# Kernel optimization log

Hardware: AMD Instinct MI355X
Metric: run time of the kernel (lower is better)

The kernel has to match this reference:

```python
import jax, jax.numpy as jnp
import numpy as np
from jax import lax

B, N, C = 16, 2304, 768
H_HEADS, D = 12, 64  # num_heads, head_dim
SCALE = 9.0 ** (-0.5)  # equivalent_head_dim ** -0.5


def setup_inputs() -> dict:
    key = jax.random.key(0)
    ks = jax.random.split(key, 8)
    return {
        "x": jax.random.normal(ks[0], (B, N, C), dtype=jnp.float32),
        "qkv_w": jax.random.normal(ks[1], (3 * C + 3 * D, C), dtype=jnp.float32) * 0.02,
        "qkv_b": jax.random.normal(ks[2], (3 * C + 3 * D,), dtype=jnp.float32) * 0.02,
        "w1": jax.random.normal(ks[3], (1, H_HEADS, D, D), dtype=jnp.float32) * 0.02,
        "w2": jax.random.normal(ks[4], (1, H_HEADS, D, D), dtype=jnp.float32) * 0.02,
        "w3": jax.random.normal(ks[5], (D, 1, 3, 3), dtype=jnp.float32) * 0.02,
        "proj_w": jax.random.normal(ks[6], (C, C + D), dtype=jnp.float32) * 0.02,
        "proj_b": jax.random.normal(ks[7], (C,), dtype=jnp.float32) * 0.02,
        "h": 48,
        "w": 48,
    }


def _inner_swiglu(k, v, w1, w2, lr=1.0):
    # k, v: [B, H, N, d]; w1, w2: [1, H, d, d]
    z1 = jnp.einsum('bhnd,hde->bhne', k, w1[0])
    z2 = jnp.einsum('bhnd,hde->bhne', k, w2[0])
    sig = jax.nn.sigmoid(z2)
    a = z2 * sig
    e = -v / float(v.shape[2]) * SCALE
    g1 = jnp.einsum('bhnd,bhne->bhde', k, e * a)
    g2 = jnp.einsum('bhnd,bhne->bhde', k, e * z1 * (sig * (1.0 + z2 * (1.0 - sig))))
    g1 = g1 / (jnp.linalg.norm(g1, axis=-2, keepdims=True) + 1.0)
    g2 = g2 / (jnp.linalg.norm(g2, axis=-2, keepdims=True) + 1.0)
    return w1 - lr * g1, w2 - lr * g2  # [B, H, d, d]


def _inner_3x3dwc(k, v, w3, hh, ww, lr=1.0):
    # k, v: [B, d, h, w]; w3: [d, 1, 3, 3]
    b, c = k.shape[0], k.shape[1]
    e = -v / float(hh * ww) * SCALE
    kp = jnp.pad(k, ((0, 0), (0, 0), (1, 1), (1, 1)))
    dots = []
    for ys in (0, 1, 2):  # 1 + dy
        for xs in (0, 1, 2):  # 1 + dx
            dots.append(jnp.sum(kp[:, :, ys:ys + hh, xs:xs + ww] * e, axis=(-2, -1)))
    g = jnp.stack(dots, axis=-1).reshape(b * c, 1, 3, 3)
    g = g / (jnp.sqrt(jnp.sum(g * g, axis=(-2, -1), keepdims=True)) + 1.0)
    return jnp.tile(w3, (b, 1, 1, 1)) - lr * g  # [B*d, 1, 3, 3]


def reference(x, qkv_w, qkv_b, w1, w2, w3, proj_w, proj_b, h, w):
    b, n, c = x.shape
    nh = w1.shape[1]
    d = c // nh
    qkv = x @ qkv_w.T + qkv_b  # [B, N, 3C + 3d]
    q1, k1, v1, q2, k2, v2 = jnp.split(
        qkv, [c, 2 * c, 3 * c, 3 * c + d, 3 * c + 2 * d], axis=-1)
    heads = lambda t: t.reshape(b, n, nh, d).transpose(0, 2, 1, 3)
    q1, k1, v1 = heads(q1), heads(k1), heads(v1)

    w1u, w2u = _inner_swiglu(k1, v1, w1, w2)
    x1 = jnp.einsum('bhnd,bhde->bhne', q1, w1u) * jax.nn.silu(
        jnp.einsum('bhnd,bhde->bhne', q1, w2u))
    x1 = x1.transpose(0, 2, 1, 3).reshape(b, n, c)

    spatial = lambda t: t.reshape(b, h, w, d).transpose(0, 3, 1, 2)  # [B, d, h, w]
    q2s, k2s, v2s = spatial(q2), spatial(k2), spatial(v2)
    w3u = _inner_3x3dwc(k2s, v2s, w3, h, w)
    x2 = lax.conv_general_dilated(
        q2s.reshape(1, b * d, h, w), w3u,
        window_strides=(1, 1), padding=((1, 1), (1, 1)),
        feature_group_count=b * d,
        dimension_numbers=('NCHW', 'OIHW', 'NCHW'))
    x2 = x2.reshape(b, d, n).transpose(0, 2, 1)  # [B, N, d]

    out = jnp.concatenate([x1, x2], axis=-1) @ proj_w.T + proj_b
    return out
```

## Files before the change

### kernel.cpp

```cpp
#include <hip/hip_runtime.h>
#include <hip/hip_bf16.h>
#include <math.h>

#define B_   16
#define N_   2304
#define C_   768
#define H_   12
#define D_   64
#define M_   (B_*N_)
#define NQKV 2496
#define NPAD 2560
#define CCP  896
#define EVS  (-1.0f/6912.0f)

typedef __bf16 bf16x8 __attribute__((ext_vector_type(8)));
typedef __bf16 bf16x4 __attribute__((ext_vector_type(4)));
typedef float  f32x4  __attribute__((ext_vector_type(4)));

static __device__ __forceinline__ void gload_lds16(const void* g, void* l) {
  __builtin_amdgcn_global_load_lds((const __attribute__((address_space(1))) void*)g,
                                   (__attribute__((address_space(3))) void*)l, 16, 0, 0);
}

static __device__ __forceinline__ bf16x8 ld8(const __bf16* p) {
  bf16x4 lo = *(const bf16x4*)p;
  bf16x4 hi = *(const bf16x4*)(p + 4);
  return __builtin_shufflevector(lo, hi, 0,1,2,3,4,5,6,7);
}

__global__ __launch_bounds__(256) void cvt_x(const float* __restrict__ in,
                                             __bf16* __restrict__ out, int n8) {
  int i = blockIdx.x * 256 + threadIdx.x;
  if (i >= n8) return;
  const float4* p = (const float4*)(in + (size_t)i * 8);
  float4 a = p[0], b = p[1];
  bf16x8 o = {(__bf16)a.x,(__bf16)a.y,(__bf16)a.z,(__bf16)a.w,
              (__bf16)b.x,(__bf16)b.y,(__bf16)b.z,(__bf16)b.w};
  *(bf16x8*)(out + (size_t)i * 8) = o;
}

__global__ __launch_bounds__(256) void cvt_wqkv(const float* __restrict__ w,
    const float* __restrict__ bias, __bf16* __restrict__ wout, float* __restrict__ bout) {
  int i = blockIdx.x * 256 + threadIdx.x;
  if (i < NPAD * 96) {
    int n = i / 96, c8 = i - n * 96;
    bf16x8 o;
    if (n < NQKV) {
      const float4* p = (const float4*)(w + (size_t)n * 768 + c8 * 8);
      float4 a = p[0], b = p[1];
      o = (bf16x8){(__bf16)a.x,(__bf16)a.y,(__bf16)a.z,(__bf16)a.w,
                   (__bf16)b.x,(__bf16)b.y,(__bf16)b.z,(__bf16)b.w};
    } else {
      o = (bf16x8){(__bf16)0.f,(__bf16)0.f,(__bf16)0.f,(__bf16)0.f,
                   (__bf16)0.f,(__bf16)0.f,(__bf16)0.f,(__bf16)0.f};
    }
    *(bf16x8*)(wout + (size_t)n * 768 + c8 * 8) = o;
  }
  if (i < NPAD) bout[i] = (i < NQKV) ? bias[i] : 0.0f;
}

__global__ __launch_bounds__(256) void cvt_pw(const float* __restrict__ in,
                                              __bf16* __restrict__ out) {
  int i = blockIdx.x * 256 + threadIdx.x;
  if (i >= 86016) return;
  int n = i / 112, c8 = i - n * 112;
  int k = c8 * 8;
  bf16x8 o;
  if (k < 832) {
    const float4* p = (const float4*)(in + (size_t)n * 832 + k);
    float4 a = p[0], b = p[1];
    o = (bf16x8){(__bf16)a.x,(__bf16)a.y,(__bf16)a.z,(__bf16)a.w,
                 (__bf16)b.x,(__bf16)b.y,(__bf16)b.z,(__bf16)b.w};
  } else {
    o = (bf16x8){(__bf16)0.f,(__bf16)0.f,(__bf16)0.f,(__bf16)0.f,
                 (__bf16)0.f,(__bf16)0.f,(__bf16)0.f,(__bf16)0.f};
  }
  *(bf16x8*)(out + (size_t)n * CCP + k) = o;
}

__global__ __launch_bounds__(256) void zeropad(__bf16* __restrict__ concat) {
  int i = blockIdx.x * 256 + threadIdx.x;
  if (i >= M_ * 8) return;
  int row = i >> 3, ch = i & 7;
  bf16x8 z = {(__bf16)0.f,(__bf16)0.f,(__bf16)0.f,(__bf16)0.f,
              (__bf16)0.f,(__bf16)0.f,(__bf16)0.f,(__bf16)0.f};
  *(bf16x8*)(concat + (size_t)row * CCP + 832 + ch * 8) = z;
}

template<int OUTF32>
__global__ __launch_bounds__(512, 2) void gemm8(
    const __bf16* __restrict__ A, const __bf16* __restrict__ Bt,
    const float* __restrict__ bias, void* __restrict__ Cout,
    const int K, const int ldc, const int nbn, const int KT)
{
  __shared__ __align__(16) __bf16 sA[2][2][128 * 64];
  __shared__ __align__(16) __bf16 sB[2][2][128 * 64];
  const int tid  = threadIdx.x;
  const int lane = tid & 63;
  const int wid  = tid >> 6;
  const int wm = wid >> 2;
  const int wn = wid & 3;
  const int l15 = lane & 15, lq = lane >> 4;

  const int nwg = gridDim.x;
  const int swz = ((int)blockIdx.x & 7) * (nwg >> 3) + ((int)blockIdx.x >> 3);
  const int bm = swz / nbn;
  const int bn = swz - bm * nbn;

  const int strow = tid >> 3;
  const int stoff = strow * 64 + (tid & 7) * 8;
  const __bf16* gA = A  + (size_t)((size_t)bm * 256 + strow) * K + ((tid & 7) ^ (strow & 7)) * 8;
  const __bf16* gB = Bt + (size_t)((size_t)bn * 256 + strow) * K + ((tid & 7) ^ (strow & 7)) * 8;

  f32x4 acc[2][4][2][2];
  #pragma unroll
  for (int a = 0; a < 2; ++a)
    #pragma unroll
    for (int m = 0; m < 4; ++m)
      #pragma unroll
      for (int b = 0; b < 2; ++b)
        #pragma unroll
        for (int n = 0; n < 2; ++n) acc[a][m][b][n] = (f32x4){0.f,0.f,0.f,0.f};

  bf16x8 af0[4][2], af1[4][2], bf0[2][2], bf1[2][2];

#define STAGE_A(q, h, T) do {                                                   \
    const size_t ko_ = (size_t)(T) * 64;                                        \
    gload_lds16(gA + (size_t)((h)*128 +  0) * K + ko_, &sA[q][h][stoff]);       \
    gload_lds16(gA + (size_t)((h)*128 + 64) * K + ko_, &sA[q][h][4096 + stoff]);\
  } while (0)
#define STAGE_B(q, h, T) do {                                                   \
    const size_t ko_ = (size_t)(T) * 64;                                        \
    gload_lds16(gB + (size_t)((h)*128 +  0) * K + ko_, &sB[q][h][stoff]);       \
    gload_lds16(gB + (size_t)((h)*128 + 64) * K + ko_, &sB[q][h][4096 + stoff]);\
  } while (0)
#define LOADA(DST, h, q) do {                                                   \
    _Pragma("unroll") for (int mf_ = 0; mf_ < 4; ++mf_) {                       \
      const int r_ = wm * 64 + mf_ * 16 + l15;                                  \
      _Pragma("unroll") for (int kk_ = 0; kk_ < 2; ++kk_)                       \
        DST[mf_][kk_] = *(const bf16x8*)&sA[q][h][r_ * 64 + (((kk_*4+lq) ^ (r_&7)) * 8)]; \
    } } while (0)
#define LOADB(DST, h, q) do {                                                   \
    _Pragma("unroll") for (int nf_ = 0; nf_ < 2; ++nf_) {                       \
      const int c_ = wn * 32 + nf_ * 16 + l15;                                  \
      _Pragma("unroll") for (int kk_ = 0; kk_ < 2; ++kk_)                       \
        DST[nf_][kk_] = *(const bf16x8*)&sB[q][h][c_ * 64 + (((kk_*4+lq) ^ (c_&7)) * 8)]; \
    } } while (0)
#define MMA(a_, b_, AF, BF) do {                                                \
    __builtin_amdgcn_s_setprio(1);                                              \
    _Pragma("unroll") for (int kk_ = 0; kk_ < 2; ++kk_)                         \
    _Pragma("unroll") for (int mf_ = 0; mf_ < 4; ++mf_)                         \
    _Pragma("unroll") for (int nf_ = 0; nf_ < 2; ++nf_)                         \
      acc[a_][mf_][b_][nf_] = __builtin_amdgcn_mfma_f32_16x16x32_bf16(          \
          AF[mf_][kk_], BF[nf_][kk_], acc[a_][mf_][b_][nf_], 0, 0, 0);          \
    __builtin_amdgcn_s_setprio(0);                                              \
  } while (0)
#define BAR  do { __builtin_amdgcn_s_barrier();                                 \
                  __builtin_amdgcn_sched_barrier(0); } while (0)
#define VMW4 do { asm volatile("s_waitcnt vmcnt(4)" ::: "memory");              \
                  __builtin_amdgcn_sched_barrier(0); } while (0)
#define VMW0 do { asm volatile("s_waitcnt vmcnt(0)" ::: "memory");              \
                  __builtin_amdgcn_sched_barrier(0); } while (0)

  STAGE_A(0, 0, 0); STAGE_A(0, 1, 0); STAGE_B(0, 0, 0); STAGE_B(0, 1, 0);
  STAGE_B(1, 0, 1);
  STAGE_A(1, 1, 1);
  VMW4;
  BAR;

  for (int t = 0; t < KT; t += 2) {
    LOADA(af0, 0, 0); LOADB(bf0, 0, 0);
    STAGE_A(1, 0, t + 1); STAGE_B(1, 1, t + 1);
    BAR; MMA(0, 0, af0, bf0); BAR;
    LOADA(af1, 1, 0);
    BAR; MMA(1, 0, af1, bf0); BAR;
    LOADB(bf1, 1, 0);
    if (t + 2 < KT) STAGE_B(0, 0, t + 2);
    BAR; MMA(1, 1, af1, bf1); BAR;
    if (t + 2 < KT) STAGE_A(0, 1, t + 2);
    BAR; MMA(0, 1, af0, bf1);
    if (t + 2 < KT) { VMW4; } else { VMW0; }
    BAR;
    LOADA(af0, 0, 1); LOADB(bf0, 0, 1);
    if (t + 2 < KT) { STAGE_A(0, 0, t + 2); STAGE_B(0, 1, t + 2); }
    BAR; MMA(0, 0, af0, bf0); BAR;
    LOADA(af1, 1, 1);
    BAR; MMA(1, 0, af1, bf0); BAR;
    LOADB(bf1, 1, 1);
    if (t + 3 < KT) STAGE_B(1, 0, t + 3);
    BAR; MMA(1, 1, af1, bf1); BAR;
    if (t + 3 < KT) STAGE_A(1, 1, t + 3);
    BAR; MMA(0, 1, af0, bf1);
    if (t + 3 < KT) { VMW4; } else { VMW0; }
    BAR;
  }
#undef STAGE_A
#undef STAGE_B
#undef LOADA
#undef LOADB
#undef MMA

  #pragma unroll
  for (int b = 0; b < 2; ++b)
    #pragma unroll
    for (int nf = 0; nf < 2; ++nf) {
      const int col = bn * 256 + b * 128 + wn * 32 + nf * 16 + l15;
      const float bs = bias[col];
      #pragma unroll
      for (int a = 0; a < 2; ++a)
        #pragma unroll
        for (int mf = 0; mf < 4; ++mf) {
          const int row0 = bm * 256 + a * 128 + wm * 64 + mf * 16 + lq * 4;
          #pragma unroll
          for (int r = 0; r < 4; ++r) {
            float v = acc[a][mf][b][nf][r] + bs;
            if (OUTF32) ((float*)Cout)[(size_t)(row0 + r) * ldc + col] = v;
            else        ((__bf16*)Cout)[(size_t)(row0 + r) * ldc + col] = (__bf16)v;
          }
        }
    }
}

__global__ __launch_bounds__(512, 1) void inner_swiglu(
    const __bf16* __restrict__ qkv, const float* __restrict__ w1,
    const float* __restrict__ w2, __bf16* __restrict__ concat)
{
  const int bh = blockIdx.x;
  const int b = bh / H_, h = bh - b * H_;
  const int tid = threadIdx.x, wid = tid >> 6, lane = tid & 63;
  const int grp = wid >> 2;
  const int wid2 = wid & 3;
  const int wr = wid2 >> 1, wc = wid2 & 1, l15 = lane & 15, lq = lane >> 4;

  __shared__ __bf16 w1T[64 * 72], w2T[64 * 72];
  __shared__ union U {
    struct { __bf16 kN[2][64 * 72], kT[2][64 * 72], vN[2][64 * 72],
                    t1T[2][64 * 72], t2T[2][64 * 72]; } c;
    struct { float g1[64 * 65], g2[64 * 65]; float nrm1[64], nrm2[64]; } g;
  } u;

  const float* w1p = w1 + h * 4096;
  const float* w2p = w2 + h * 4096;
  for (int idx = tid; idx < 4096; idx += 512) {
    int d = idx >> 6, e = idx & 63;
    w1T[e * 72 + d] = (__bf16)w1p[idx];
    w2T[e * 72 + d] = (__bf16)w2p[idx];
  }

  f32x4 g1a[2][2], g2a[2][2];
  #pragma unroll
  for (int i = 0; i < 2; ++i)
    #pragma unroll
    for (int j = 0; j < 2; ++j) { g1a[i][j] = (f32x4){0.f,0.f,0.f,0.f}; g2a[i][j] = (f32x4){0.f,0.f,0.f,0.f}; }

  const size_t rowb = (size_t)b * N_;
  const int koff = C_ + h * D_;
  const int voff = 2 * C_ + h * D_;
  const int st = tid & 255, sn = st >> 2, sdb = st & 3;

  for (int it = 0; it < 18; ++it) {
    const int n0 = (it * 2 + grp) * 64;
    {
      const __bf16* src = qkv + (rowb + n0 + sn) * (size_t)NPAD + koff + sdb * 16;
      bf16x8 va = *(const bf16x8*)src;
      bf16x8 vb = *(const bf16x8*)(src + 8);
      __bf16* kn = &u.c.kN[grp][sn * 72 + sdb * 16];
      *(bf16x4*)(kn + 0)  = __builtin_shufflevector(va, va, 0,1,2,3);
      *(bf16x4*)(kn + 4)  = __builtin_shufflevector(va, va, 4,5,6,7);
      *(bf16x4*)(kn + 8)  = __builtin_shufflevector(vb, vb, 0,1,2,3);
      *(bf16x4*)(kn + 12) = __builtin_shufflevector(vb, vb, 4,5,6,7);
      #pragma unroll
      for (int j = 0; j < 8; ++j) u.c.kT[grp][(sdb * 16 + j) * 72 + sn] = va[j];
      #pragma unroll
      for (int j = 0; j < 8; ++j) u.c.kT[grp][(sdb * 16 + 8 + j) * 72 + sn] = vb[j];
      const __bf16* vsrc = qkv + (rowb + n0 + sn) * (size_t)NPAD + voff + sdb * 16;
      bf16x8 wa = *(const bf16x8*)vsrc;
      bf16x8 wb = *(const bf16x8*)(vsrc + 8);
      __bf16* vn = &u.c.vN[grp][sn * 72 + sdb * 16];
      *(bf16x4*)(vn + 0)  = __builtin_shufflevector(wa, wa, 0,1,2,3);
      *(bf16x4*)(vn + 4)  = __builtin_shufflevector(wa, wa, 4,5,6,7);
      *(bf16x4*)(vn + 8)  = __builtin_shufflevector(wb, wb, 0,1,2,3);
      *(bf16x4*)(vn + 12) = __builtin_shufflevector(wb, wb, 4,5,6,7);
    }
    __syncthreads();

    f32x4 z1[2][2], z2[2][2];
    #pragma unroll
    for (int i = 0; i < 2; ++i)
      #pragma unroll
      for (int j = 0; j < 2; ++j) { z1[i][j] = (f32x4){0.f,0.f,0.f,0.f}; z2[i][j] = (f32x4){0.f,0.f,0.f,0.f}; }
    #pragma unroll
    for (int kk = 0; kk < 2; ++kk) {
      bf16x8 af[2], b1[2], b2[2];
      #pragma unroll
      for (int mi = 0; mi < 2; ++mi)
        af[mi] = ld8(&u.c.kN[grp][(wr * 32 + mi * 16 + l15) * 72 + kk * 32 + lq * 8]);
      #pragma unroll
      for (int ni = 0; ni < 2; ++ni) {
        int e = wc * 32 + ni * 16 + l15;
        b1[ni] = ld8(&w1T[e * 72 + kk * 32 + lq * 8]);
        b2[ni] = ld8(&w2T[e * 72 + kk * 32 + lq * 8]);
      }
      #pragma unroll
      for (int mi = 0; mi < 2; ++mi)
        #pragma unroll
        for (int ni = 0; ni < 2; ++ni) {
          z1[mi][ni] = __builtin_amdgcn_mfma_f32_16x16x32_bf16(af[mi], b1[ni], z1[mi][ni], 0, 0, 0);
          z2[mi][ni] = __builtin_amdgcn_mfma_f32_16x16x32_bf16(af[mi], b2[ni], z2[mi][ni], 0, 0, 0);
        }
    }

    #pragma unroll
    for (int mi = 0; mi < 2; ++mi)
      #pragma unroll
      for (int ni = 0; ni < 2; ++ni) {
        int nl = wr * 32 + mi * 16 + lq * 4;
        int e  = wc * 32 + ni * 16 + l15;
        #pragma unroll
        for (int r = 0; r < 4; ++r) {
          float vv  = (float)u.c.vN[grp][(nl + r) * 72 + e];
          float ev  = vv * EVS;
          float z1v = z1[mi][ni][r], z2v = z2[mi][ni][r];
          float sg  = 1.0f / (1.0f + __expf(-z2v));
          float t1  = ev * (z2v * sg);
          float t2  = ev * z1v * (sg * (1.0f + z2v * (1.0f - sg)));
          u.c.t1T[grp][e * 72 + nl + r] = (__bf16)t1;
          u.c.t2T[grp][e * 72 + nl + r] = (__bf16)t2;
        }
      }
    __syncthreads();

    #pragma unroll
    for (int kk = 0; kk < 2; ++kk) {
      bf16x8 af[2], b1[2], b2[2];
      #pragma unroll
      for (int mi = 0; mi < 2; ++mi)
        af[mi] = ld8(&u.c.kT[grp][(wr * 32 + mi * 16 + l15) * 72 + kk * 32 + lq * 8]);
      #pragma unroll
      for (int ni = 0; ni < 2; ++ni) {
        int e = wc * 32 + ni * 16 + l15;
        b1[ni] = ld8(&u.c.t1T[grp][e * 72 + kk * 32 + lq * 8]);
        b2[ni] = ld8(&u.c.t2T[grp][e * 72 + kk * 32 + lq * 8]);
      }
      #pragma unroll
      for (int mi = 0; mi < 2; ++mi)
        #pragma unroll
        for (int ni = 0; ni < 2; ++ni) {
          g1a[mi][ni] = __builtin_amdgcn_mfma_f32_16x16x32_bf16(af[mi], b1[ni], g1a[mi][ni], 0, 0, 0);
          g2a[mi][ni] = __builtin_amdgcn_mfma_f32_16x16x32_bf16(af[mi], b2[ni], g2a[mi][ni], 0, 0, 0);
        }
    }
    __syncthreads();
  }

  if (grp == 0) {
    #pragma unroll
    for (int mi = 0; mi < 2; ++mi)
      #pragma unroll
      for (int ni = 0; ni < 2; ++ni)
        #pragma unroll
        for (int r = 0; r < 4; ++r) {
          int d = wr * 32 + mi * 16 + lq * 4 + r;
          int e = wc * 32 + ni * 16 + l15;
          u.g.g1[d * 65 + e] = g1a[mi][ni][r];
          u.g.g2[d * 65 + e] = g2a[mi][ni][r];
        }
  }
  __syncthreads();
  if (grp == 1) {
    #pragma unroll
    for (int mi = 0; mi < 2; ++mi)
      #pragma unroll
      for (int ni = 0; ni < 2; ++ni)
        #pragma unroll
        for (int r = 0; r < 4; ++r) {
          int d = wr * 32 + mi * 16 + lq * 4 + r;
          int e = wc * 32 + ni * 16 + l15;
          u.g.g1[d * 65 + e] += g1a[mi][ni][r];
          u.g.g2[d * 65 + e] += g2a[mi][ni][r];
        }
  }
  __syncthreads();
  if (tid < 128) {
    const float* gs = (tid < 64) ? u.g.g1 : u.g.g2;
    int e = tid & 63;
    float s = 0.f;
    for (int d = 0; d < 64; ++d) { float gv = gs[d * 65 + e]; s += gv * gv; }
    float rn = 1.0f / (sqrtf(s) + 1.0f);
    if (tid < 64) u.g.nrm1[e] = rn; else u.g.nrm2[e] = rn;
  }
  __syncthreads();
  for (int idx = tid; idx < 4096; idx += 512) {
    int d = idx >> 6, e = idx & 63;
    float wu1 = w1p[idx] - u.g.g1[d * 65 + e] * u.g.nrm1[e];
    float wu2 = w2p[idx] - u.g.g2[d * 65 + e] * u.g.nrm2[e];
    w1T[e * 72 + d] = (__bf16)wu1;
    w2T[e * 72 + d] = (__bf16)wu2;
  }
  __syncthreads();

  const int qoff = h * D_;
  for (int it = 0; it < 18; ++it) {
    const int n0 = (it * 2 + grp) * 64;
    {
      const __bf16* src = qkv + (rowb + n0 + sn) * (size_t)NPAD + qoff + sdb * 16;
      bf16x8 va = *(const bf16x8*)src;
      bf16x8 vb = *(const bf16x8*)(src + 8);
      __bf16* kn = &u.c.kN[grp][sn * 72 + sdb * 16];
      *(bf16x4*)(kn + 0)  = __builtin_shufflevector(va, va, 0,1,2,3);
      *(bf16x4*)(kn + 4)  = __builtin_shufflevector(va, va, 4,5,6,7);
      *(bf16x4*)(kn + 8)  = __builtin_shufflevector(vb, vb, 0,1,2,3);
      *(bf16x4*)(kn + 12) = __builtin_shufflevector(vb, vb, 4,5,6,7);
    }
    __syncthreads();
    f32x4 y1[2][2], y2[2][2];
    #pragma unroll
    for (int i = 0; i < 2; ++i)
      #pragma unroll
      for (int j = 0; j < 2; ++j) { y1[i][j] = (f32x4){0.f,0.f,0.f,0.f}; y2[i][j] = (f32x4){0.f,0.f,0.f,0.f}; }
    #pragma unroll
    for (int kk = 0; kk < 2; ++kk) {
      bf16x8 af[2], b1[2], b2[2];
      #pragma unroll
      for (int mi = 0; mi < 2; ++mi)
        af[mi] = ld8(&u.c.kN[grp][(wr * 32 + mi * 16 + l15) * 72 + kk * 32 + lq * 8]);
      #pragma unroll
      for (int ni = 0; ni < 2; ++ni) {
        int e = wc * 32 + ni * 16 + l15;
        b1[ni] = ld8(&w1T[e * 72 + kk * 32 + lq * 8]);
        b2[ni] = ld8(&w2T[e * 72 + kk * 32 + lq * 8]);
      }
      #pragma unroll
      for (int mi = 0; mi < 2; ++mi)
        #pragma unroll
        for (int ni = 0; ni < 2; ++ni) {
          y1[mi][ni] = __builtin_amdgcn_mfma_f32_16x16x32_bf16(af[mi], b1[ni], y1[mi][ni], 0, 0, 0);
          y2[mi][ni] = __builtin_amdgcn_mfma_f32_16x16x32_bf16(af[mi], b2[ni], y2[mi][ni], 0, 0, 0);
        }
    }
    #pragma unroll
    for (int mi = 0; mi < 2; ++mi)
      #pragma unroll
      for (int ni = 0; ni < 2; ++ni) {
        int nl = wr * 32 + mi * 16 + lq * 4;
        int e  = wc * 32 + ni * 16 + l15;
        #pragma unroll
        for (int r = 0; r < 4; ++r) {
          float a1 = y1[mi][ni][r], a2 = y2[mi][ni][r];
          float sg = 1.0f / (1.0f + __expf(-a2));
          concat[(rowb + n0 + nl + r) * (size_t)CCP + h * D_ + e] = (__bf16)(a1 * (a2 * sg));
        }
      }
    __syncthreads();
  }
}

__global__ __launch_bounds__(256) void dwc_grad2(const __bf16* __restrict__ qkv,
                                                 float* __restrict__ w3p) {
  const int blk = blockIdx.x;
  const int b = blk / 12, sp = blk - b * 12;
  const int tid = threadIdx.x, dd = tid & 63, rl = tid >> 6;
  __shared__ __bf16 kS[6 * 50 * 64];
  __shared__ float red[4][9][64];
  for (int i = tid; i < 9600; i += 256) ((unsigned*)kS)[i] = 0u;
  __syncthreads();
  const size_t base = (size_t)b * N_ * NPAD;
  for (int i = tid; i < 6 * 48 * 8; i += 256) {
    int y6 = i / 384; int rem = i - y6 * 384; int x = rem >> 3; int c8 = rem & 7;
    int y = 4 * sp - 1 + y6;
    if (y >= 0 && y < 48) {
      int p = y * 48 + x;
      bf16x8 v = *(const bf16x8*)&qkv[base + (size_t)p * NPAD + 2368 + c8 * 8];
      *(bf16x8*)&kS[((y6 * 50) + x + 1) * 64 + c8 * 8] = v;
    }
  }
  __syncthreads();
  float acc[9];
  #pragma unroll
  for (int j = 0; j < 9; ++j) acc[j] = 0.f;
  const int y = 4 * sp + rl;
  for (int x = 0; x < 48; ++x) {
    int p = y * 48 + x;
    float e = (float)qkv[base + (size_t)p * NPAD + 2432 + dd] * EVS;
    #pragma unroll
    for (int j = 0; j < 9; ++j) {
      int ys = j / 3, xs = j - ys * 3;
      acc[j] += (float)kS[((rl + ys) * 50 + x + xs) * 64 + dd] * e;
    }
  }
  #pragma unroll
  for (int j = 0; j < 9; ++j) red[rl][j][dd] = acc[j];
  __syncthreads();
  if (rl == 0) {
    #pragma unroll
    for (int j = 0; j < 9; ++j) {
      float s = red[0][j][dd] + red[1][j][dd] + red[2][j][dd] + red[3][j][dd];
      w3p[((size_t)(b * 12 + sp) * 64 + dd) * 9 + j] = s;
    }
  }
}

__global__ __launch_bounds__(256) void dwc_upd(const float* __restrict__ w3p,
    const float* __restrict__ w3, float* __restrict__ w3u) {
  int i = blockIdx.x * 256 + threadIdx.x;
  if (i >= 1024) return;
  int b = i >> 6, dd = i & 63;
  float g[9];
  #pragma unroll
  for (int j = 0; j < 9; ++j) g[j] = 0.f;
  for (int sp = 0; sp < 12; ++sp)
    #pragma unroll
    for (int j = 0; j < 9; ++j)
      g[j] += w3p[((size_t)(b * 12 + sp) * 64 + dd) * 9 + j];
  float ss = 0.f;
  #pragma unroll
  for (int j = 0; j < 9; ++j) ss += g[j] * g[j];
  float rn = 1.0f / (sqrtf(ss) + 1.0f);
  #pragma unroll
  for (int j = 0; j < 9; ++j) w3u[i * 9 + j] = w3[dd * 9 + j] - g[j] * rn;
}

__global__ __launch_bounds__(256) void dwc_apply2(const __bf16* __restrict__ qkv,
    const float* __restrict__ w3u, __bf16* __restrict__ concat) {
  const int blk = blockIdx.x;
  const int b = blk / 12, sp = blk - b * 12;
  const int tid = threadIdx.x, dd = tid & 63, rl = tid >> 6;
  __shared__ __bf16 qS[6 * 50 * 64];
  for (int i = tid; i < 9600; i += 256) ((unsigned*)qS)[i] = 0u;
  __syncthreads();
  const size_t base = (size_t)b * N_ * NPAD;
  for (int i = tid; i < 6 * 48 * 8; i += 256) {
    int y6 = i / 384; int rem = i - y6 * 384; int x = rem >> 3; int c8 = rem & 7;
    int y = 4 * sp - 1 + y6;
    if (y >= 0 && y < 48) {
      int p = y * 48 + x;
      bf16x8 v = *(const bf16x8*)&qkv[base + (size_t)p * NPAD + 2304 + c8 * 8];
      *(bf16x8*)&qS[((y6 * 50) + x + 1) * 64 + c8 * 8] = v;
    }
  }
  __syncthreads();
  float wv[9];
  #pragma unroll
  for (int j = 0; j < 9; ++j) wv[j] = w3u[(size_t)(b * 64 + dd) * 9 + j];
  const int y = 4 * sp + rl;
  for (int x = 0; x < 48; ++x) {
    float s = 0.f;
    #pragma unroll
    for (int j = 0; j < 9; ++j) {
      int ys = j / 3, xs = j - ys * 3;
      s += (float)qS[((rl + ys) * 50 + x + xs) * 64 + dd] * wv[j];
    }
    int p = y * 48 + x;
    concat[((size_t)b * N_ + p) * CCP + 768 + dd] = (__bf16)s;
  }
}

extern "C" void kernel_launch(void* const* d_in, const int* in_sizes, int n_in,
                              void* d_out, int out_size, void* d_ws, size_t ws_size,
                              hipStream_t stream) {
  const float* x      = (const float*)d_in[0];
  const float* qkv_w  = (const float*)d_in[1];
  const float* qkv_b  = (const float*)d_in[2];
  const float* w1     = (const float*)d_in[3];
  const float* w2     = (const float*)d_in[4];
  const float* w3     = (const float*)d_in[5];
  const float* proj_w = (const float*)d_in[6];
  const float* proj_b = (const float*)d_in[7];

  char* ws = (char*)d_ws;
  __bf16* xb     = (__bf16*)ws;
  __bf16* wqkvb  = (__bf16*)(ws + 56623104);
  float*  qkvbp  = (float*) (ws + 60555264);
  __bf16* concat = (__bf16*)ws;
  __bf16* qkvb16 = (__bf16*)(ws + 66060288);
  __bf16* pwb    = (__bf16*)(ws + 254803968);
  float*  w3u    = (float*) (ws + 256180224);
  float*  w3p    = (float*) (ws + 256217088);

  cvt_x   <<<13824, 256, 0, stream>>>(x, xb, 3538944);
  cvt_wqkv<<<  960, 256, 0, stream>>>(qkv_w, qkv_b, wqkvb, qkvbp);
  cvt_pw  <<<  336, 256, 0, stream>>>(proj_w, pwb);

  gemm8<0><<<1440, 512, 0, stream>>>(xb, wqkvb, qkvbp, (void*)qkvb16,
                                     768, NPAD, 10, 12);

  zeropad<<<1152, 256, 0, stream>>>(concat);
  inner_swiglu<<<192, 512, 0, stream>>>(qkvb16, w1, w2, concat);
  dwc_grad2 <<<192, 256, 0, stream>>>(qkvb16, w3p);
  dwc_upd   <<<  4, 256, 0, stream>>>(w3p, w3, w3u);
  dwc_apply2<<<192, 256, 0, stream>>>(qkvb16, w3u, concat);

  gemm8<1><<<432, 512, 0, stream>>>(concat, pwb, proj_b, d_out,
                                    CCP, 768, 3, 14);
}
```

Baseline: 453.2 us.

## Replace 256x256 ping-pong GEMM with simpler 128x128 double-buffered GEMM

Swaps the 8-wave 256x256-tile GEMM, which had an interleaved ping-pong schedule of barriers, priorities and partial waits, for a 4-wave 128x128-tile kernel. The new kernel uses a plain double-buffered LDS loop that prefetches the next K-tile and waits with vmcnt(0) before each barrier. Launching four times as many workgroups should give better occupancy and wave balance across CUs. In exchange it loses data reuse per tile, doubling global and LDS traffic per FLOP, and it drops the fine-grained overlap of loads and MFMA.

```diff
diff --git a/kernel.cpp b/kernel.cpp
--- a/kernel.cpp
+++ b/kernel.cpp
@@ -88,18 +88,17 @@
 }
 
 template<int OUTF32>
-__global__ __launch_bounds__(512, 2) void gemm8(
+__global__ __launch_bounds__(256, 2) void gemmP(
     const __bf16* __restrict__ A, const __bf16* __restrict__ Bt,
     const float* __restrict__ bias, void* __restrict__ Cout,
     const int K, const int ldc, const int nbn, const int KT)
 {
-  __shared__ __align__(16) __bf16 sA[2][2][128 * 64];
-  __shared__ __align__(16) __bf16 sB[2][2][128 * 64];
+  __shared__ __align__(16) __bf16 sA[2][128 * 64];
+  __shared__ __align__(16) __bf16 sB[2][128 * 64];
   const int tid  = threadIdx.x;
   const int lane = tid & 63;
   const int wid  = tid >> 6;
-  const int wm = wid >> 2;
-  const int wn = wid & 3;
+  const int wm = wid >> 1, wn = wid & 1;
   const int l15 = lane & 15, lq = lane >> 4;
 
   const int nwg = gridDim.x;
@@ -109,116 +108,75 @@
 
   const int strow = tid >> 3;
   const int stoff = strow * 64 + (tid & 7) * 8;
-  const __bf16* gA = A  + (size_t)((size_t)bm * 256 + strow) * K + ((tid & 7) ^ (strow & 7)) * 8;
-  const __bf16* gB = Bt + (size_t)((size_t)bn * 256 + strow) * K + ((tid & 7) ^ (strow & 7)) * 8;
-
-  f32x4 acc[2][4][2][2];
-  #pragma unroll
-  for (int a = 0; a < 2; ++a)
-    #pragma unroll
-    for (int m = 0; m < 4; ++m)
-      #pragma unroll
-      for (int b = 0; b < 2; ++b)
-        #pragma unroll
-        for (int n = 0; n < 2; ++n) acc[a][m][b][n] = (f32x4){0.f,0.f,0.f,0.f};
-
-  bf16x8 af0[4][2], af1[4][2], bf0[2][2], bf1[2][2];
-
-#define STAGE_A(q, h, T) do {                                                   \
+  const __bf16* gA = A  + (size_t)((size_t)bm * 128 + strow) * K + ((tid & 7) ^ (strow & 7)) * 8;
+  const __bf16* gB = Bt + (size_t)((size_t)bn * 128 + strow) * K + ((tid & 7) ^ (strow & 7)) * 8;
+
+  f32x4 acc[4][4];
+  #pragma unroll
+  for (int m = 0; m < 4; ++m)
+    #pragma unroll
+    for (int n = 0; n < 4; ++n) acc[m][n] = (f32x4){0.f,0.f,0.f,0.f};
+
+#define STAGE(q, T) do {                                                        \
     const size_t ko_ = (size_t)(T) * 64;                                        \
-    gload_lds16(gA + (size_t)((h)*128 +  0) * K + ko_, &sA[q][h][stoff]);       \
-    gload_lds16(gA + (size_t)((h)*128 + 64) * K + ko_, &sA[q][h][4096 + stoff]);\
-  } while (0)
-#define STAGE_B(q, h, T) do {                                                   \
-    const size_t ko_ = (size_t)(T) * 64;                                        \
-    gload_lds16(gB + (size_t)((h)*128 +  0) * K + ko_, &sB[q][h][stoff]);       \
-    gload_lds16(gB + (size_t)((h)*128 + 64) * K + ko_, &sB[q][h][4096 + stoff]);\
-  } while (0)
-#define LOADA(DST, h, q) do {                                                   \
-    _Pragma("unroll") for (int mf_ = 0; mf_ < 4; ++mf_) {                       \
-      const int r_ = wm * 64 + mf_ * 16 + l15;                                  \
-      _Pragma("unroll") for (int kk_ = 0; kk_ < 2; ++kk_)                       \
-        DST[mf_][kk_] = *(const bf16x8*)&sA[q][h][r_ * 64 + (((kk_*4+lq) ^ (r_&7)) * 8)]; \
+    _Pragma("unroll")                                                           \
+    for (int j_ = 0; j_ < 4; ++j_) {                                            \
+      gload_lds16(gA + (size_t)(j_ * 32) * K + ko_, &sA[q][j_ * 2048 + stoff]); \
+      gload_lds16(gB + (size_t)(j_ * 32) * K + ko_, &sB[q][j_ * 2048 + stoff]); \
     } } while (0)
-#define LOADB(DST, h, q) do {                                                   \
-    _Pragma("unroll") for (int nf_ = 0; nf_ < 2; ++nf_) {                       \
-      const int c_ = wn * 32 + nf_ * 16 + l15;                                  \
-      _Pragma("unroll") for (int kk_ = 0; kk_ < 2; ++kk_)                       \
-        DST[nf_][kk_] = *(const bf16x8*)&sB[q][h][c_ * 64 + (((kk_*4+lq) ^ (c_&7)) * 8)]; \
-    } } while (0)
-#define MMA(a_, b_, AF, BF) do {                                                \
-    __builtin_amdgcn_s_setprio(1);                                              \
-    _Pragma("unroll") for (int kk_ = 0; kk_ < 2; ++kk_)                         \
-    _Pragma("unroll") for (int mf_ = 0; mf_ < 4; ++mf_)                         \
-    _Pragma("unroll") for (int nf_ = 0; nf_ < 2; ++nf_)                         \
-      acc[a_][mf_][b_][nf_] = __builtin_amdgcn_mfma_f32_16x16x32_bf16(          \
-          AF[mf_][kk_], BF[nf_][kk_], acc[a_][mf_][b_][nf_], 0, 0, 0);          \
-    __builtin_amdgcn_s_setprio(0);                                              \
-  } while (0)
-#define BAR  do { __builtin_amdgcn_s_barrier();                                 \
-                  __builtin_amdgcn_sched_barrier(0); } while (0)
-#define VMW4 do { asm volatile("s_waitcnt vmcnt(4)" ::: "memory");              \
-                  __builtin_amdgcn_sched_barrier(0); } while (0)
-#define VMW0 do { asm volatile("s_waitcnt vmcnt(0)" ::: "memory");              \
-                  __builtin_amdgcn_sched_barrier(0); } while (0)
-
-  STAGE_A(0, 0, 0); STAGE_A(0, 1, 0); STAGE_B(0, 0, 0); STAGE_B(0, 1, 0);
-  STAGE_B(1, 0, 1);
-  STAGE_A(1, 1, 1);
-  VMW4;
-  BAR;
-
-  for (int t = 0; t < KT; t += 2) {
-    LOADA(af0, 0, 0); LOADB(bf0, 0, 0);
-    STAGE_A(1, 0, t + 1); STAGE_B(1, 1, t + 1);
-    BAR; MMA(0, 0, af0, bf0); BAR;
-    LOADA(af1, 1, 0);
-    BAR; MMA(1, 0, af1, bf0); BAR;
-    LOADB(bf1, 1, 0);
-    if (t + 2 < KT) STAGE_B(0, 0, t + 2);
-    BAR; MMA(1, 1, af1, bf1); BAR;
-    if (t + 2 < KT) STAGE_A(0, 1, t + 2);
-    BAR; MMA(0, 1, af0, bf1);
-    if (t + 2 < KT) { VMW4; } else { VMW0; }
-    BAR;
-    LOADA(af0, 0, 1); LOADB(bf0, 0, 1);
-    if (t + 2 < KT) { STAGE_A(0, 0, t + 2); STAGE_B(0, 1, t + 2); }
-    BAR; MMA(0, 0, af0, bf0); BAR;
-    LOADA(af1, 1, 1);
-    BAR; MMA(1, 0, af1, bf0); BAR;
-    LOADB(bf1, 1, 1);
-    if (t + 3 < KT) STAGE_B(1, 0, t + 3);
-    BAR; MMA(1, 1, af1, bf1); BAR;
-    if (t + 3 < KT) STAGE_A(1, 1, t + 3);
-    BAR; MMA(0, 1, af0, bf1);
-    if (t + 3 < KT) { VMW4; } else { VMW0; }
-    BAR;
-  }
-#undef STAGE_A
-#undef STAGE_B
-#undef LOADA
-#undef LOADB
-#undef MMA
-
-  #pragma unroll
-  for (int b = 0; b < 2; ++b)
-    #pragma unroll
-    for (int nf = 0; nf < 2; ++nf) {
-      const int col = bn * 256 + b * 128 + wn * 32 + nf * 16 + l15;
-      const float bs = bias[col];
-      #pragma unroll
-      for (int a = 0; a < 2; ++a)
-        #pragma unroll
-        for (int mf = 0; mf < 4; ++mf) {
-          const int row0 = bm * 256 + a * 128 + wm * 64 + mf * 16 + lq * 4;
-          #pragma unroll
-          for (int r = 0; r < 4; ++r) {
-            float v = acc[a][mf][b][nf][r] + bs;
-            if (OUTF32) ((float*)Cout)[(size_t)(row0 + r) * ldc + col] = v;
-            else        ((__bf16*)Cout)[(size_t)(row0 + r) * ldc + col] = (__bf16)v;
-          }
-        }
-    }
+
+  STAGE(0, 0);
+  asm volatile("s_waitcnt vmcnt(0)" ::: "memory");
+  __builtin_amdgcn_s_barrier();
+
+  for (int t = 0; t < KT; ++t) {
+    const int q = t & 1;
+    if (t + 1 < KT) STAGE(q ^ 1, t + 1);
+
+    bf16x8 af[4][2], bf[4][2];
+    #pragma unroll
+    for (int mf = 0; mf < 4; ++mf) {
+      const int r = wm * 64 + mf * 16 + l15;
+      #pragma unroll
+      for (int kk = 0; kk < 2; ++kk)
+        af[mf][kk] = *(const bf16x8*)&sA[q][r * 64 + (((kk * 4 + lq) ^ (r & 7)) * 8)];
+    }
+    #pragma unroll
+    for (int nf = 0; nf < 4; ++nf) {
+      const int c = wn * 64 + nf * 16 + l15;
+      #pragma unroll
+      for (int kk = 0; kk < 2; ++kk)
+        bf[nf][kk] = *(const bf16x8*)&sB[q][c * 64 + (((kk * 4 + lq) ^ (c & 7)) * 8)];
+    }
+    #pragma unroll
+    for (int kk = 0; kk < 2; ++kk)
+      #pragma unroll
+      for (int mf = 0; mf < 4; ++mf)
+        #pragma unroll
+        for (int nf = 0; nf < 4; ++nf)
+          acc[mf][nf] = __builtin_amdgcn_mfma_f32_16x16x32_bf16(
+              af[mf][kk], bf[nf][kk], acc[mf][nf], 0, 0, 0);
+
+    if (t + 1 < KT) asm volatile("s_waitcnt vmcnt(0)" ::: "memory");
+    __builtin_amdgcn_s_barrier();
+  }
+#undef STAGE
+
+  #pragma unroll
+  for (int nf = 0; nf < 4; ++nf) {
+    const int col = bn * 128 + wn * 64 + nf * 16 + l15;
+    const float bs = bias[col];
+    #pragma unroll
+    for (int mf = 0; mf < 4; ++mf) {
+      const int row0 = bm * 128 + wm * 64 + mf * 16 + lq * 4;
+      #pragma unroll
+      for (int r = 0; r < 4; ++r) {
+        float v = acc[mf][nf][r] + bs;
+        if (OUTF32) ((float*)Cout)[(size_t)(row0 + r) * ldc + col] = v;
+        else        ((__bf16*)Cout)[(size_t)(row0 + r) * ldc + col] = (__bf16)v;
+      }
+    }
+  }
 }
 
 __global__ __launch_bounds__(512, 1) void inner_swiglu(
@@ -581,8 +539,8 @@
   cvt_wqkv<<<  960, 256, 0, stream>>>(qkv_w, qkv_b, wqkvb, qkvbp);
   cvt_pw  <<<  336, 256, 0, stream>>>(proj_w, pwb);
 
-  gemm8<0><<<1440, 512, 0, stream>>>(xb, wqkvb, qkvbp, (void*)qkvb16,
-                                     768, NPAD, 10, 12);
+  gemmP<0><<<5760, 256, 0, stream>>>(xb, wqkvb, qkvbp, (void*)qkvb16,
+                                     768, NPAD, 20, 12);
 
   zeropad<<<1152, 256, 0, stream>>>(concat);
   inner_swiglu<<<192, 512, 0, stream>>>(qkvb16, w1, w2, concat);
@@ -590,6 +548,6 @@
   dwc_upd   <<<  4, 256, 0, stream>>>(w3p, w3, w3u);
   dwc_apply2<<<192, 256, 0, stream>>>(qkvb16, w3u, concat);
 
-  gemm8<1><<<432, 512, 0, stream>>>(concat, pwb, proj_b, d_out,
-                                    CCP, 768, 3, 14);
-}
+  gemmP<1><<<1728, 256, 0, stream>>>(concat, pwb, proj_b, d_out,
+                                     CCP, 768, 6, 14);
+}
```

Result: slower. 471.9 us (+4.1%).

## Split inner SwiGLU into grad/update/apply kernels and relax GEMM barrier scheduling

Applied to the files above, without the earlier changes.

Replaces the single 192-block inner_swiglu kernel with three kernels: a 768-block gradient pass that writes per-segment partial gradients to workspace, a small reduction/normalise/update kernel, and a 1152-block apply kernel. This spreads the work across many more blocks, up from one block per (batch, head), and shrinks LDS use so several blocks can share a CU. V is now read straight from global memory instead of being staged in LDS. The cost is extra global traffic for the partial gradients and updated weights, plus two more launches. In the GEMM, sched_barrier fences are dropped from the barrier and vmcnt macros and explicit lgkmcnt waits are placed before each MFMA group, giving the compiler more scheduling freedom.

```diff
diff --git a/kernel.cpp b/kernel.cpp
--- a/kernel.cpp
+++ b/kernel.cpp
@@ -155,12 +155,11 @@
           AF[mf_][kk_], BF[nf_][kk_], acc[a_][mf_][b_][nf_], 0, 0, 0);          \
     __builtin_amdgcn_s_setprio(0);                                              \
   } while (0)
-#define BAR  do { __builtin_amdgcn_s_barrier();                                 \
+#define BAR  __builtin_amdgcn_s_barrier()
+#define LGKM do { asm volatile("s_waitcnt lgkmcnt(0)" ::: "memory");            \
                   __builtin_amdgcn_sched_barrier(0); } while (0)
-#define VMW4 do { asm volatile("s_waitcnt vmcnt(4)" ::: "memory");              \
-                  __builtin_amdgcn_sched_barrier(0); } while (0)
-#define VMW0 do { asm volatile("s_waitcnt vmcnt(0)" ::: "memory");              \
-                  __builtin_amdgcn_sched_barrier(0); } while (0)
+#define VMW4 asm volatile("s_waitcnt vmcnt(4)" ::: "memory")
+#define VMW0 asm volatile("s_waitcnt vmcnt(0)" ::: "memory")
 
   STAGE_A(0, 0, 0); STAGE_A(0, 1, 0); STAGE_B(0, 0, 0); STAGE_B(0, 1, 0);
   STAGE_B(1, 0, 1);
@@ -171,24 +170,24 @@
   for (int t = 0; t < KT; t += 2) {
     LOADA(af0, 0, 0); LOADB(bf0, 0, 0);
     STAGE_A(1, 0, t + 1); STAGE_B(1, 1, t + 1);
-    BAR; MMA(0, 0, af0, bf0); BAR;
+    BAR; LGKM; MMA(0, 0, af0, bf0); BAR;
     LOADA(af1, 1, 0);
-    BAR; MMA(1, 0, af1, bf0); BAR;
+    BAR; LGKM; MMA(1, 0, af1, bf0); BAR;
     LOADB(bf1, 1, 0);
     if (t + 2 < KT) STAGE_B(0, 0, t + 2);
-    BAR; MMA(1, 1, af1, bf1); BAR;
+    BAR; LGKM; MMA(1, 1, af1, bf1); BAR;
     if (t + 2 < KT) STAGE_A(0, 1, t + 2);
     BAR; MMA(0, 1, af0, bf1);
     if (t + 2 < KT) { VMW4; } else { VMW0; }
     BAR;
     LOADA(af0, 0, 1); LOADB(bf0, 0, 1);
     if (t + 2 < KT) { STAGE_A(0, 0, t + 2); STAGE_B(0, 1, t + 2); }
-    BAR; MMA(0, 0, af0, bf0); BAR;
+    BAR; LGKM; MMA(0, 0, af0, bf0); BAR;
     LOADA(af1, 1, 1);
-    BAR; MMA(1, 0, af1, bf0); BAR;
+    BAR; LGKM; MMA(1, 0, af1, bf0); BAR;
     LOADB(bf1, 1, 1);
     if (t + 3 < KT) STAGE_B(1, 0, t + 3);
-    BAR; MMA(1, 1, af1, bf1); BAR;
+    BAR; LGKM; MMA(1, 1, af1, bf1); BAR;
     if (t + 3 < KT) STAGE_A(1, 1, t + 3);
     BAR; MMA(0, 1, af0, bf1);
     if (t + 3 < KT) { VMW4; } else { VMW0; }
@@ -221,27 +220,23 @@
     }
 }
 
-__global__ __launch_bounds__(512, 1) void inner_swiglu(
+__global__ __launch_bounds__(256, 3) void inner_grad(
     const __bf16* __restrict__ qkv, const float* __restrict__ w1,
-    const float* __restrict__ w2, __bf16* __restrict__ concat)
+    const float* __restrict__ w2, float* __restrict__ gpart)
 {
-  const int bh = blockIdx.x;
+  const int blk = blockIdx.x;
+  const int bh = blk >> 2, seg = blk & 3;
   const int b = bh / H_, h = bh - b * H_;
   const int tid = threadIdx.x, wid = tid >> 6, lane = tid & 63;
-  const int grp = wid >> 2;
-  const int wid2 = wid & 3;
-  const int wr = wid2 >> 1, wc = wid2 & 1, l15 = lane & 15, lq = lane >> 4;
+  const int wr = wid >> 1, wc = wid & 1, l15 = lane & 15, lq = lane >> 4;
 
   __shared__ __bf16 w1T[64 * 72], w2T[64 * 72];
-  __shared__ union U {
-    struct { __bf16 kN[2][64 * 72], kT[2][64 * 72], vN[2][64 * 72],
-                    t1T[2][64 * 72], t2T[2][64 * 72]; } c;
-    struct { float g1[64 * 65], g2[64 * 65]; float nrm1[64], nrm2[64]; } g;
-  } u;
+  __shared__ __bf16 kNt1[64 * 72];
+  __shared__ __bf16 kT[64 * 72], t2T[64 * 72];
 
   const float* w1p = w1 + h * 4096;
   const float* w2p = w2 + h * 4096;
-  for (int idx = tid; idx < 4096; idx += 512) {
+  for (int idx = tid; idx < 4096; idx += 256) {
     int d = idx >> 6, e = idx & 63;
     w1T[e * 72 + d] = (__bf16)w1p[idx];
     w2T[e * 72 + d] = (__bf16)w2p[idx];
@@ -256,31 +251,24 @@
   const size_t rowb = (size_t)b * N_;
   const int koff = C_ + h * D_;
   const int voff = 2 * C_ + h * D_;
-  const int st = tid & 255, sn = st >> 2, sdb = st & 3;
-
-  for (int it = 0; it < 18; ++it) {
-    const int n0 = (it * 2 + grp) * 64;
+  const int sn = tid >> 2, sdb = tid & 3;
+  __syncthreads();
+
+  for (int ci = 0; ci < 9; ++ci) {
+    const int n0 = seg * 576 + ci * 64;
     {
       const __bf16* src = qkv + (rowb + n0 + sn) * (size_t)NPAD + koff + sdb * 16;
       bf16x8 va = *(const bf16x8*)src;
       bf16x8 vb = *(const bf16x8*)(src + 8);
-      __bf16* kn = &u.c.kN[grp][sn * 72 + sdb * 16];
+      __bf16* kn = &kNt1[sn * 72 + sdb * 16];
       *(bf16x4*)(kn + 0)  = __builtin_shufflevector(va, va, 0,1,2,3);
       *(bf16x4*)(kn + 4)  = __builtin_shufflevector(va, va, 4,5,6,7);
       *(bf16x4*)(kn + 8)  = __builtin_shufflevector(vb, vb, 0,1,2,3);
       *(bf16x4*)(kn + 12) = __builtin_shufflevector(vb, vb, 4,5,6,7);
       #pragma unroll
-      for (int j = 0; j < 8; ++j) u.c.kT[grp][(sdb * 16 + j) * 72 + sn] = va[j];
-      #pragma unroll
-      for (int j = 0; j < 8; ++j) u.c.kT[grp][(sdb * 16 + 8 + j) * 72 + sn] = vb[j];
-      const __bf16* vsrc = qkv + (rowb + n0 + sn) * (size_t)NPAD + voff + sdb * 16;
-      bf16x8 wa = *(const bf16x8*)vsrc;
-      bf16x8 wb = *(const bf16x8*)(vsrc + 8);
-      __bf16* vn = &u.c.vN[grp][sn * 72 + sdb * 16];
-      *(bf16x4*)(vn + 0)  = __builtin_shufflevector(wa, wa, 0,1,2,3);
-      *(bf16x4*)(vn + 4)  = __builtin_shufflevector(wa, wa, 4,5,6,7);
-      *(bf16x4*)(vn + 8)  = __builtin_shufflevector(wb, wb, 0,1,2,3);
-      *(bf16x4*)(vn + 12) = __builtin_shufflevector(wb, wb, 4,5,6,7);
+      for (int j = 0; j < 8; ++j) kT[(sdb * 16 + j) * 72 + sn] = va[j];
+      #pragma unroll
+      for (int j = 0; j < 8; ++j) kT[(sdb * 16 + 8 + j) * 72 + sn] = vb[j];
     }
     __syncthreads();
 
@@ -294,7 +282,7 @@
       bf16x8 af[2], b1[2], b2[2];
       #pragma unroll
       for (int mi = 0; mi < 2; ++mi)
-        af[mi] = ld8(&u.c.kN[grp][(wr * 32 + mi * 16 + l15) * 72 + kk * 32 + lq * 8]);
+        af[mi] = ld8(&kNt1[(wr * 32 + mi * 16 + l15) * 72 + kk * 32 + lq * 8]);
       #pragma unroll
       for (int ni = 0; ni < 2; ++ni) {
         int e = wc * 32 + ni * 16 + l15;
@@ -309,6 +297,7 @@
           z2[mi][ni] = __builtin_amdgcn_mfma_f32_16x16x32_bf16(af[mi], b2[ni], z2[mi][ni], 0, 0, 0);
         }
     }
+    __syncthreads();
 
     #pragma unroll
     for (int mi = 0; mi < 2; ++mi)
@@ -316,16 +305,17 @@
       for (int ni = 0; ni < 2; ++ni) {
         int nl = wr * 32 + mi * 16 + lq * 4;
         int e  = wc * 32 + ni * 16 + l15;
+        const __bf16* vp = qkv + (rowb + n0 + nl) * (size_t)NPAD + voff + e;
         #pragma unroll
         for (int r = 0; r < 4; ++r) {
-          float vv  = (float)u.c.vN[grp][(nl + r) * 72 + e];
+          float vv  = (float)vp[(size_t)r * NPAD];
           float ev  = vv * EVS;
           float z1v = z1[mi][ni][r], z2v = z2[mi][ni][r];
           float sg  = 1.0f / (1.0f + __expf(-z2v));
           float t1  = ev * (z2v * sg);
           float t2  = ev * z1v * (sg * (1.0f + z2v * (1.0f - sg)));
-          u.c.t1T[grp][e * 72 + nl + r] = (__bf16)t1;
-          u.c.t2T[grp][e * 72 + nl + r] = (__bf16)t2;
+          kNt1[e * 72 + nl + r] = (__bf16)t1;
+          t2T [e * 72 + nl + r] = (__bf16)t2;
         }
       }
     __syncthreads();
@@ -335,12 +325,12 @@
       bf16x8 af[2], b1[2], b2[2];
       #pragma unroll
       for (int mi = 0; mi < 2; ++mi)
-        af[mi] = ld8(&u.c.kT[grp][(wr * 32 + mi * 16 + l15) * 72 + kk * 32 + lq * 8]);
+        af[mi] = ld8(&kT[(wr * 32 + mi * 16 + l15) * 72 + kk * 32 + lq * 8]);
       #pragma unroll
       for (int ni = 0; ni < 2; ++ni) {
         int e = wc * 32 + ni * 16 + l15;
-        b1[ni] = ld8(&u.c.t1T[grp][e * 72 + kk * 32 + lq * 8]);
-        b2[ni] = ld8(&u.c.t2T[grp][e * 72 + kk * 32 + lq * 8]);
+        b1[ni] = ld8(&kNt1[e * 72 + kk * 32 + lq * 8]);
+        b2[ni] = ld8(&t2T [e * 72 + kk * 32 + lq * 8]);
       }
       #pragma unroll
       for (int mi = 0; mi < 2; ++mi)
@@ -353,60 +343,89 @@
     __syncthreads();
   }
 
-  if (grp == 0) {
-    #pragma unroll
-    for (int mi = 0; mi < 2; ++mi)
-      #pragma unroll
-      for (int ni = 0; ni < 2; ++ni)
-        #pragma unroll
-        for (int r = 0; r < 4; ++r) {
-          int d = wr * 32 + mi * 16 + lq * 4 + r;
-          int e = wc * 32 + ni * 16 + l15;
-          u.g.g1[d * 65 + e] = g1a[mi][ni][r];
-          u.g.g2[d * 65 + e] = g2a[mi][ni][r];
-        }
-  }
-  __syncthreads();
-  if (grp == 1) {
-    #pragma unroll
-    for (int mi = 0; mi < 2; ++mi)
-      #pragma unroll
-      for (int ni = 0; ni < 2; ++ni)
-        #pragma unroll
-        for (int r = 0; r < 4; ++r) {
-          int d = wr * 32 + mi * 16 + lq * 4 + r;
-          int e = wc * 32 + ni * 16 + l15;
-          u.g.g1[d * 65 + e] += g1a[mi][ni][r];
-          u.g.g2[d * 65 + e] += g2a[mi][ni][r];
-        }
+  float* gp = gpart + (size_t)blk * 8192;
+  #pragma unroll
+  for (int mi = 0; mi < 2; ++mi)
+    #pragma unroll
+    for (int ni = 0; ni < 2; ++ni)
+      #pragma unroll
+      for (int r = 0; r < 4; ++r) {
+        int d = wr * 32 + mi * 16 + lq * 4 + r;
+        int e = wc * 32 + ni * 16 + l15;
+        gp[d * 64 + e]        = g1a[mi][ni][r];
+        gp[4096 + d * 64 + e] = g2a[mi][ni][r];
+      }
+}
+
+__global__ __launch_bounds__(256) void inner_upd(
+    const float* __restrict__ gpart, const float* __restrict__ w1,
+    const float* __restrict__ w2, __bf16* __restrict__ wu)
+{
+  const int bh = blockIdx.x;
+  const int h = bh % H_;
+  const int tid = threadIdx.x;
+  __shared__ float g1[64 * 65], g2[64 * 65];
+  __shared__ float nrm1[64], nrm2[64];
+  const float* w1p = w1 + h * 4096;
+  const float* w2p = w2 + h * 4096;
+
+  for (int idx = tid; idx < 4096; idx += 256) {
+    float s1 = 0.f, s2 = 0.f;
+    #pragma unroll
+    for (int s = 0; s < 4; ++s) {
+      const float* gp = gpart + (size_t)(bh * 4 + s) * 8192;
+      s1 += gp[idx]; s2 += gp[4096 + idx];
+    }
+    int d = idx >> 6, e = idx & 63;
+    g1[d * 65 + e] = s1; g2[d * 65 + e] = s2;
   }
   __syncthreads();
   if (tid < 128) {
-    const float* gs = (tid < 64) ? u.g.g1 : u.g.g2;
+    const float* gs = (tid < 64) ? g1 : g2;
     int e = tid & 63;
     float s = 0.f;
     for (int d = 0; d < 64; ++d) { float gv = gs[d * 65 + e]; s += gv * gv; }
     float rn = 1.0f / (sqrtf(s) + 1.0f);
-    if (tid < 64) u.g.nrm1[e] = rn; else u.g.nrm2[e] = rn;
-  }
-  __syncthreads();
-  for (int idx = tid; idx < 4096; idx += 512) {
+    if (tid < 64) nrm1[e] = rn; else nrm2[e] = rn;
+  }
+  __syncthreads();
+  __bf16* wub = wu + (size_t)bh * 8192;
+  for (int idx = tid; idx < 4096; idx += 256) {
     int d = idx >> 6, e = idx & 63;
-    float wu1 = w1p[idx] - u.g.g1[d * 65 + e] * u.g.nrm1[e];
-    float wu2 = w2p[idx] - u.g.g2[d * 65 + e] * u.g.nrm2[e];
-    w1T[e * 72 + d] = (__bf16)wu1;
-    w2T[e * 72 + d] = (__bf16)wu2;
-  }
-  __syncthreads();
-
+    wub[idx]        = (__bf16)(w1p[idx] - g1[d * 65 + e] * nrm1[e]);
+    wub[4096 + idx] = (__bf16)(w2p[idx] - g2[d * 65 + e] * nrm2[e]);
+  }
+}
+
+__global__ __launch_bounds__(256) void inner_apply(
+    const __bf16* __restrict__ qkv, const __bf16* __restrict__ wu,
+    __bf16* __restrict__ concat)
+{
+  const int blk = blockIdx.x;
+  const int bh = blk / 6, seg = blk - bh * 6;
+  const int b = bh / H_, h = bh - b * H_;
+  const int tid = threadIdx.x, wid = tid >> 6, lane = tid & 63;
+  const int wr = wid >> 1, wc = wid & 1, l15 = lane & 15, lq = lane >> 4;
+
+  __shared__ __bf16 w1T[64 * 72], w2T[64 * 72], qN[64 * 72];
+  const __bf16* wub = wu + (size_t)bh * 8192;
+  for (int idx = tid; idx < 4096; idx += 256) {
+    int d = idx >> 6, e = idx & 63;
+    w1T[e * 72 + d] = wub[idx];
+    w2T[e * 72 + d] = wub[4096 + idx];
+  }
+
+  const size_t rowb = (size_t)b * N_;
   const int qoff = h * D_;
-  for (int it = 0; it < 18; ++it) {
-    const int n0 = (it * 2 + grp) * 64;
+  const int sn = tid >> 2, sdb = tid & 3;
+
+  for (int ci = 0; ci < 6; ++ci) {
+    const int n0 = seg * 384 + ci * 64;
     {
       const __bf16* src = qkv + (rowb + n0 + sn) * (size_t)NPAD + qoff + sdb * 16;
       bf16x8 va = *(const bf16x8*)src;
       bf16x8 vb = *(const bf16x8*)(src + 8);
-      __bf16* kn = &u.c.kN[grp][sn * 72 + sdb * 16];
+      __bf16* kn = &qN[sn * 72 + sdb * 16];
       *(bf16x4*)(kn + 0)  = __builtin_shufflevector(va, va, 0,1,2,3);
       *(bf16x4*)(kn + 4)  = __builtin_shufflevector(va, va, 4,5,6,7);
       *(bf16x4*)(kn + 8)  = __builtin_shufflevector(vb, vb, 0,1,2,3);
@@ -423,7 +442,7 @@
       bf16x8 af[2], b1[2], b2[2];
       #pragma unroll
       for (int mi = 0; mi < 2; ++mi)
-        af[mi] = ld8(&u.c.kN[grp][(wr * 32 + mi * 16 + l15) * 72 + kk * 32 + lq * 8]);
+        af[mi] = ld8(&qN[(wr * 32 + mi * 16 + l15) * 72 + kk * 32 + lq * 8]);
       #pragma unroll
       for (int ni = 0; ni < 2; ++ni) {
         int e = wc * 32 + ni * 16 + l15;
@@ -576,6 +595,8 @@
   __bf16* pwb    = (__bf16*)(ws + 254803968);
   float*  w3u    = (float*) (ws + 256180224);
   float*  w3p    = (float*) (ws + 256217088);
+  float*  gpart  = (float*) (ws + 256659456);
+  __bf16* wu     = (__bf16*)(ws + 281825280);
 
   cvt_x   <<<13824, 256, 0, stream>>>(x, xb, 3538944);
   cvt_wqkv<<<  960, 256, 0, stream>>>(qkv_w, qkv_b, wqkvb, qkvbp);
@@ -585,7 +606,9 @@
                                      768, NPAD, 10, 12);
 
   zeropad<<<1152, 256, 0, stream>>>(concat);
-  inner_swiglu<<<192, 512, 0, stream>>>(qkvb16, w1, w2, concat);
+  inner_grad <<< 768, 256, 0, stream>>>(qkvb16, w1, w2, gpart);
+  inner_upd  <<< 192, 256, 0, stream>>>(gpart, w1, w2, wu);
+  inner_apply<<<1152, 256, 0, stream>>>(qkvb16, wu, concat);
   dwc_grad2 <<<192, 256, 0, stream>>>(qkvb16, w3p);
   dwc_upd   <<<  4, 256, 0, stream>>>(w3p, w3, w3u);
   dwc_apply2<<<192, 256, 0, stream>>>(qkvb16, w3u, concat);
```

Result: faster. 442.9 us (-2.3%).
